# Kernel tuning notes

Measured on AMD Instinct MI355X. Metric: run time of the kernel, lower is better.

The kernel has to match this reference:

```python
import jax, jax.numpy as jnp
import numpy as np

B, E, K, S, D, H, C = 8192, 8, 2, 32, 3072, 256, 100  # batch, experts, fix_points, img size, flat dim, hidden, classes


def setup_inputs() -> dict:
    key = jax.random.key(0)
    ks = jax.random.split(key, 6)
    return {
        "x": jax.random.normal(ks[0], (B, 3, S, S), jnp.float32),
        "coeffs_t": jax.random.uniform(ks[1], (K,), jnp.float32),
        "router_w": jax.random.normal(ks[2], (K, D, E), jnp.float32) * 0.02,
        "router_b": jnp.zeros((K, E), jnp.float32),
        "w1": jax.random.normal(ks[3], (E, K, D, H), jnp.float32) * 0.02,
        "b1": jnp.zeros((E, K, H), jnp.float32),
        "w2": jax.random.normal(ks[4], (E, K, H, C), jnp.float32) * 0.02,
        "b2": jnp.zeros((E, K, C), jnp.float32),
    }


def reference(x, coeffs_t, router_w, router_b, w1, b1, w2, b2):
    xf = x.reshape(x.shape[0], -1)  # [B, D]
    # Curve parameter blend: W = sum_k coeffs_t[k] * W_k (CurveParameter semantics)
    Wr = jnp.einsum('k,kde->de', coeffs_t, router_w)
    br = jnp.einsum('k,ke->e', coeffs_t, router_b)
    # Router: top-1 expert index per sample
    idx = jnp.argmax(xf @ Wr + br, axis=-1)  # [B] int
    # Blended expert weights
    W1 = jnp.einsum('k,ekdh->edh', coeffs_t, w1)
    B1 = jnp.einsum('k,ekh->eh', coeffs_t, b1)
    W2 = jnp.einsum('k,ekhc->ehc', coeffs_t, w2)
    B2 = jnp.einsum('k,ekc->ec', coeffs_t, b2)
    # Expert MLP (computed for all experts with static shapes, then top-1 gather;
    # identical math to torch's boolean-mask dispatch/scatter)
    h = jax.nn.gelu(jnp.einsum('bd,edh->beh', xf, W1) + B1, approximate=False)  # [B,E,H]
    o = jnp.einsum('beh,ehc->bec', h, W2) + B2  # [B,E,C]
    return jnp.take_along_axis(o, idx[:, None, None], axis=1)[:, 0, :]  # [B,C]
```

## Files before the change

kernel.cpp:

```cpp
#include <hip/hip_runtime.h>
#include <math.h>

#define B_  8192
#define E_  8
#define D_  3072
#define H_  256
#define C_  100
#define DH_ (D_*H_)
#define HC_ (H_*C_)
#define KS_ 8
#define KSEG_ (D_/KS_)
#define RKS_ 16
#define RSEG_ (D_/RKS_)
#define RB_ (B_/256)
#define NTMAX_ 136
#define NT2MAX_ 528

#define MEGA_R_   (RB_*RKS_)
#define MEGA_W1_  (24*4*8)
#define MEGA_W2_  (C_*E_)
#define MEGA_BB_  3
#define MEGA_TOT_ (MEGA_R_ + MEGA_W1_ + MEGA_W2_ + MEGA_BB_)

typedef __attribute__((ext_vector_type(4))) float  f32x4;
typedef __attribute__((ext_vector_type(8))) __bf16 bf16x8;
typedef __attribute__((ext_vector_type(8))) unsigned short ush8;
typedef __attribute__((ext_vector_type(4))) unsigned short ush4;

__device__ inline unsigned short bf16_rne(float f) {
    unsigned u = __builtin_bit_cast(unsigned, f);
    unsigned r = (u + 0x7FFFu + ((u >> 16) & 1u)) >> 16;
    return (unsigned short)r;
}
__device__ inline float bf16_f(unsigned short h) {
    unsigned u = ((unsigned)h) << 16;
    return __builtin_bit_cast(float, u);
}

#define MISC_B1_ (E_*H_/4)
#define MISC_B2_ (E_*C_/4)

__global__ __launch_bounds__(256) void mega_k(
        const float* __restrict__ x, const float* __restrict__ rw,
        const float* __restrict__ w1, const float* __restrict__ w2,
        const float* __restrict__ b1, const float* __restrict__ b2,
        unsigned short* __restrict__ Whi, unsigned short* __restrict__ Wlo,
        unsigned short* __restrict__ W2thi, unsigned short* __restrict__ W2tlo,
        float* __restrict__ B1b, float* __restrict__ B2b,
        double* __restrict__ lpart, const float* __restrict__ coeffs) {
    __shared__ char smem[36864];
    int bid = blockIdx.x;
    int t = threadIdx.x;

    if (bid < MEGA_R_) {
        float  (*xs)[64][33] = (float(*)[64][33])smem;
        double (*wls)[8]     = (double(*)[8])(smem + 33792);
        int w = t >> 6, lane = t & 63;
        int rowblk = (bid & (RB_ - 1)) * 256;
        int s2     = bid >> 5;
        int kbase  = s2 * RSEG_;
        int row0   = rowblk + w * 64;
        double c0 = (double)coeffs[0], c1 = (double)coeffs[1];

        double acc[8] = {0, 0, 0, 0, 0, 0, 0, 0};

        float4 px[8];
        float rwa[4], rwb[4];
        #pragma unroll
        for (int it = 0; it < 8; it++) {
            int i = lane + it * 64;
            int r = i >> 3, c4 = i & 7;
            px[it] = *(const float4*)(x + (size_t)(row0 + r) * D_ + kbase + c4 * 4);
        }
        if (w == 0) {
            #pragma unroll
            for (int it = 0; it < 4; it++) {
                int i = lane + it * 64;
                int k = i >> 3, ee = i & 7;
                rwa[it] = rw[(size_t)(kbase + k) * 8 + ee];
                rwb[it] = rw[(size_t)(D_ + kbase + k) * 8 + ee];
            }
        }

        for (int kb = 0; kb < RSEG_; kb += 32) {
            #pragma unroll
            for (int it = 0; it < 8; it++) {
                int i = lane + it * 64;
                int r = i >> 3, c4 = i & 7;
                *(float4*)&xs[w][r][c4 * 4] = px[it];
            }
            if (w == 0) {
                #pragma unroll
                for (int it = 0; it < 4; it++) {
                    int i = lane + it * 64;
                    int k = i >> 3, ee = i & 7;
                    wls[k][ee] = c0 * (double)rwa[it] + c1 * (double)rwb[it];
                }
            }
            __syncthreads();

            if (kb + 32 < RSEG_) {
                #pragma unroll
                for (int it = 0; it < 8; it++) {
                    int i = lane + it * 64;
                    int r = i >> 3, c4 = i & 7;
                    px[it] = *(const float4*)(x + (size_t)(row0 + r) * D_ +
                                              kbase + kb + 32 + c4 * 4);
                }
                if (w == 0) {
                    #pragma unroll
                    for (int it = 0; it < 4; it++) {
                        int i = lane + it * 64;
                        int k = i >> 3, ee = i & 7;
                        rwa[it] = rw[(size_t)(kbase + kb + 32 + k) * 8 + ee];
                        rwb[it] = rw[(size_t)(D_ + kbase + kb + 32 + k) * 8 + ee];
                    }
                }
            }

            #pragma unroll
            for (int kk = 0; kk < 32; kk++) {
                double xv = (double)xs[w][lane][kk];
                double2 w01 = *(const double2*)&wls[kk][0];
                double2 w23 = *(const double2*)&wls[kk][2];
                double2 w45 = *(const double2*)&wls[kk][4];
                double2 w67 = *(const double2*)&wls[kk][6];
                acc[0] = fma(xv, w01.x, acc[0]);
                acc[1] = fma(xv, w01.y, acc[1]);
                acc[2] = fma(xv, w23.x, acc[2]);
                acc[3] = fma(xv, w23.y, acc[3]);
                acc[4] = fma(xv, w45.x, acc[4]);
                acc[5] = fma(xv, w45.y, acc[5]);
                acc[6] = fma(xv, w67.x, acc[6]);
                acc[7] = fma(xv, w67.y, acc[7]);
            }
            __syncthreads();
        }
        size_t base = ((size_t)s2 * B_ + row0 + lane) * 8;
        #pragma unroll
        for (int ee = 0; ee < 8; ee++) lpart[base + ee] = acc[ee];

    } else if (bid < MEGA_R_ + MEGA_W1_) {
        int lid = bid - MEGA_R_;
        int e  = lid / 96;
        int r  = lid - e * 96;
        int h0 = (r / 24) * 64;
        int d0 = (r % 24) * 128;
        const int TP = 136;
        unsigned short* thi = (unsigned short*)smem;
        unsigned short* tlo = thi + 64 * TP;
        float c0 = coeffs[0], c1 = coeffs[1];
        int h = t & 63, dl = t >> 6;
        const float* pa = w1 + ((size_t)(e * 2 + 0) * D_ + d0) * H_ + h0 + h;
        const float* pb = w1 + ((size_t)(e * 2 + 1) * D_ + d0) * H_ + h0 + h;
        #pragma unroll 8
        for (int it = 0; it < 32; it++) {
            int d = it * 4 + dl;
            float v = c0 * pa[(size_t)d * H_] + c1 * pb[(size_t)d * H_];
            unsigned short hi = bf16_rne(v);
            thi[h * TP + d] = hi;
            tlo[h * TP + d] = bf16_rne(v - bf16_f(hi));
        }
        __syncthreads();
        #pragma unroll
        for (int it = 0; it < 4; it++) {
            int i = t + it * 256;
            int hh = i >> 4, d8 = (i & 15) * 8;
            size_t g = (size_t)(e * H_ + h0 + hh) * D_ + d0 + d8;
            *(ush8*)(Whi + g) = *(const ush8*)&thi[hh * TP + d8];
            *(ush8*)(Wlo + g) = *(const ush8*)&tlo[hh * TP + d8];
        }

    } else if (bid < MEGA_R_ + MEGA_W1_ + MEGA_W2_) {
        int lid = bid - (MEGA_R_ + MEGA_W1_);
        int c = lid % C_, e = lid / C_;
        int k = t;
        float c0 = coeffs[0], c1 = coeffs[1];
        float v = c0 * w2[((size_t)(e * 2 + 0) * H_ + k) * C_ + c]
                + c1 * w2[((size_t)(e * 2 + 1) * H_ + k) * C_ + c];
        unsigned short hi = bf16_rne(v);
        W2thi[(size_t)(e * C_ + c) * H_ + k] = hi;
        W2tlo[(size_t)(e * C_ + c) * H_ + k] = bf16_rne(v - bf16_f(hi));

    } else {
        int gid = (bid - (MEGA_R_ + MEGA_W1_ + MEGA_W2_)) * 256 + t;
        float c0 = coeffs[0], c1 = coeffs[1];
        if (gid < MISC_B1_) {
            const float4* p = (const float4*)b1;
            int e = gid / (H_ / 4), r = gid - e * (H_ / 4);
            float4 a = p[(e * 2 + 0) * (H_ / 4) + r];
            float4 bq = p[(e * 2 + 1) * (H_ / 4) + r];
            float4 o;
            o.x = c0 * a.x + c1 * bq.x;
            o.y = c0 * a.y + c1 * bq.y;
            o.z = c0 * a.z + c1 * bq.z;
            o.w = c0 * a.w + c1 * bq.w;
            ((float4*)B1b)[gid] = o;
        } else if (gid < MISC_B1_ + MISC_B2_) {
            int g2 = gid - MISC_B1_;
            const float4* p = (const float4*)b2;
            int e = g2 / (C_ / 4), r = g2 - e * (C_ / 4);
            float4 a = p[(e * 2 + 0) * (C_ / 4) + r];
            float4 bq = p[(e * 2 + 1) * (C_ / 4) + r];
            float4 o;
            o.x = c0 * a.x + c1 * bq.x;
            o.y = c0 * a.y + c1 * bq.y;
            o.z = c0 * a.z + c1 * bq.z;
            o.w = c0 * a.w + c1 * bq.w;
            ((float4*)B2b)[g2] = o;
        }
    }
}

__global__ __launch_bounds__(256) void argmax_hist_k(
        const double* __restrict__ lpart, const float* __restrict__ rb,
        const float* __restrict__ coeffs, int* __restrict__ idx,
        int* __restrict__ hist) {
    __shared__ int scnt[8];
    int t = threadIdx.x;
    if (t < 8) scnt[t] = 0;
    __syncthreads();
    int b = blockIdx.x * 256 + t;
    double c0 = (double)coeffs[0], c1 = (double)coeffs[1];
    double l[8];
    #pragma unroll
    for (int e = 0; e < 8; e++)
        l[e] = c0 * (double)rb[e] + c1 * (double)rb[8 + e];
    for (int s2 = 0; s2 < RKS_; s2++) {
        const double2* pp = (const double2*)(lpart + ((size_t)s2 * B_ + b) * 8);
        double2 v0 = pp[0], v1 = pp[1], v2 = pp[2], v3 = pp[3];
        l[0] += v0.x; l[1] += v0.y; l[2] += v1.x; l[3] += v1.y;
        l[4] += v2.x; l[5] += v2.y; l[6] += v3.x; l[7] += v3.y;
    }
    double best = -1e300;
    int bi = 0;
    #pragma unroll
    for (int e = 0; e < 8; e++)
        if (l[e] > best) { best = l[e]; bi = e; }
    idx[b] = bi;
    atomicAdd(&scnt[bi], 1);
    __syncthreads();
    if (t < 8) hist[blockIdx.x * 8 + t] = scnt[t];
}

__global__ __launch_bounds__(256) void scatter2_k(
        const int* __restrict__ idx, const int* __restrict__ hist,
        int* __restrict__ order, int* __restrict__ cnt, int* __restrict__ off,
        int* __restrict__ tmap, int* __restrict__ tmap2, int* __restrict__ ntl) {
    __shared__ int sbi[256];
    __shared__ int stot[8];
    __shared__ int sbase[8];
    int b0 = blockIdx.x, t = threadIdx.x;
    int b = b0 * 256 + t;
    int mybi = idx[b];
    sbi[t] = mybi;
    if (t < 8) {
        int tot = 0, pre = 0;
        for (int bb = 0; bb < RB_; bb++) {
            int h = hist[bb * 8 + t];
            if (bb < b0) pre += h;
            tot += h;
        }
        stot[t] = tot;
        sbase[t] = pre;
    }
    __syncthreads();
    if (t < 8) {
        int o = 0;
        for (int j = 0; j < t; j++) o += stot[j];
        sbase[t] += o;
    }
    __syncthreads();
    int rank = 0;
    for (int i = 0; i < 256; i++) {
        int v = sbi[i];
        rank += (i < t && v == mybi) ? 1 : 0;
    }
    order[sbase[mybi] + rank] = (mybi << 16) | b;

    if (b0 == 0 && t == 0) {
        int s = 0;
        for (int e = 0; e < E_; e++) { cnt[e] = stot[e]; off[e] = s; s += stot[e]; }
        int nt = 0;
        for (int e = 0; e < E_; e++)
            for (int t0 = 0; t0 < stot[e]; t0 += 64)
                tmap[nt++] = (e << 16) | t0;
        ntl[0] = nt;
        int nt2 = 0;
        for (int e = 0; e < E_; e++)
            for (int t0 = 0; t0 < stot[e]; t0 += 16)
                tmap2[nt2++] = (e << 16) | t0;
        ntl[1] = nt2;
    }
}

template<int MODE>
__global__ __launch_bounds__(256, 3) void gemm1_t(
        const float* __restrict__ x, const unsigned short* __restrict__ Whi,
        const unsigned short* __restrict__ Wlo, const int* __restrict__ order,
        const int* __restrict__ cnt, const int* __restrict__ off,
        const int* __restrict__ tmap, const int* __restrict__ ntl,
        float* __restrict__ dst) {
    int tid = blockIdx.y;
    if (tid >= ntl[0]) return;
    int tm = tmap[tid];
    int e = tm >> 16, tile0 = tm & 0xFFFF;
    int ce = cnt[e];
    int s = blockIdx.x;

    __shared__ int rows[64];
    __shared__ unsigned short xs_hi[64 * 40];
    __shared__ unsigned short xs_lo[64 * 40];
    __shared__ unsigned short ws_hi[256 * 40];
    __shared__ unsigned short ws_lo[256 * 40];

    int t = threadIdx.x;
    if (t < 64) {
        int i = tile0 + t;
        rows[t] = (i < ce) ? (order[off[e] + i] & 0xFFFF) : -1;
    }
    __syncthreads();
    int xrow0 = rows[0];

    int lane = t & 63, w = t >> 6;
    int lr = lane & 15, quad = lane >> 4;
    int kbase = s * KSEG_;

    f32x4 acc[4][4];
    #pragma unroll
    for (int mt = 0; mt < 4; mt++)
        #pragma unroll
        for (int nt = 0; nt < 4; nt++)
            acc[mt][nt] = (f32x4){0.f, 0.f, 0.f, 0.f};

    for (int kb = 0; kb < KSEG_; kb += 32) {
        #pragma unroll
        for (int it = 0; it < 2; it++) {
            int i = t + it * 256;
            int rr = i >> 3, sg = i & 7;
            int row = rows[rr];
            if (row < 0) row = xrow0;
            float4 v = *(const float4*)(x + (size_t)row * D_ + kbase + kb + sg * 4);
            unsigned short h4[4], l4[4];
            float vv[4] = {v.x, v.y, v.z, v.w};
            #pragma unroll
            for (int j = 0; j < 4; j++) {
                unsigned short hi = bf16_rne(vv[j]);
                h4[j] = hi;
                l4[j] = bf16_rne(vv[j] - bf16_f(hi));
            }
            *(ush4*)&xs_hi[rr * 40 + sg * 4] = *(const ush4*)h4;
            *(ush4*)&xs_lo[rr * 40 + sg * 4] = *(const ush4*)l4;
        }
        #pragma unroll
        for (int it = 0; it < 4; it++) {
            int i = t + it * 256;
            int col = i >> 2, ch = i & 3;
            size_t g = (size_t)(e * H_ + col) * D_ + kbase + kb + ch * 8;
            *(ush8*)&ws_hi[col * 40 + ch * 8] = *(const ush8*)(Whi + g);
            *(ush8*)&ws_lo[col * 40 + ch * 8] = *(const ush8*)(Wlo + g);
        }
        __syncthreads();

        bf16x8 ah[4], al[4], bh[4], bl[4];
        #pragma unroll
        for (int mt = 0; mt < 4; mt++) {
            ah[mt] = __builtin_bit_cast(bf16x8, *(const ush8*)&xs_hi[(mt * 16 + lr) * 40 + quad * 8]);
            al[mt] = __builtin_bit_cast(bf16x8, *(const ush8*)&xs_lo[(mt * 16 + lr) * 40 + quad * 8]);
        }
        #pragma unroll
        for (int nt = 0; nt < 4; nt++) {
            int col = w * 64 + nt * 16 + lr;
            bh[nt] = __builtin_bit_cast(bf16x8, *(const ush8*)&ws_hi[col * 40 + quad * 8]);
            bl[nt] = __builtin_bit_cast(bf16x8, *(const ush8*)&ws_lo[col * 40 + quad * 8]);
        }
        #pragma unroll
        for (int mt = 0; mt < 4; mt++)
            #pragma unroll
            for (int nt = 0; nt < 4; nt++) {
                acc[mt][nt] = __builtin_amdgcn_mfma_f32_16x16x32_bf16(ah[mt], bh[nt], acc[mt][nt], 0, 0, 0);
                acc[mt][nt] = __builtin_amdgcn_mfma_f32_16x16x32_bf16(al[mt], bh[nt], acc[mt][nt], 0, 0, 0);
                acc[mt][nt] = __builtin_amdgcn_mfma_f32_16x16x32_bf16(ah[mt], bl[nt], acc[mt][nt], 0, 0, 0);
                acc[mt][nt] = __builtin_amdgcn_mfma_f32_16x16x32_bf16(al[mt], bl[nt], acc[mt][nt], 0, 0, 0);
            }
        __syncthreads();
    }

    size_t p0 = (size_t)off[e] + tile0;
    if (MODE == 1) {
        float* dp = dst + ((size_t)s * B_ + p0) * H_;
        #pragma unroll
        for (int mt = 0; mt < 4; mt++) {
            int rl = mt * 16 + quad * 4;
            #pragma unroll
            for (int nt = 0; nt < 4; nt++) {
                int col = w * 64 + nt * 16 + lr;
                #pragma unroll
                for (int rg = 0; rg < 4; rg++) {
                    if (tile0 + rl + rg < ce)
                        dp[(size_t)(rl + rg) * H_ + col] = acc[mt][nt][rg];
                }
            }
        }
    } else {
        #pragma unroll
        for (int mt = 0; mt < 4; mt++) {
            int rl = mt * 16 + quad * 4;
            #pragma unroll
            for (int nt = 0; nt < 4; nt++) {
                int col = w * 64 + nt * 16 + lr;
                #pragma unroll
                for (int rg = 0; rg < 4; rg++) {
                    if (tile0 + rl + rg < ce)
                        atomicAdd(&dst[(p0 + rl + rg) * H_ + col], acc[mt][nt][rg]);
                }
            }
        }
    }
}

__global__ __launch_bounds__(256) void bias_gelu_k(
        float* __restrict__ hws, const float* __restrict__ B1b,
        const int* __restrict__ order) {
    int gid = blockIdx.x * 256 + threadIdx.x;
    int p = gid >> 6, c4 = (gid & 63) * 4;
    int e = order[p] >> 16;
    float4 v = *(const float4*)(hws + (size_t)p * H_ + c4);
    const float4 bb = *(const float4*)(B1b + e * H_ + c4);
    float pre[4] = {v.x + bb.x, v.y + bb.y, v.z + bb.z, v.w + bb.w};
    float4 o;
    o.x = 0.5f * pre[0] * (1.0f + erff(pre[0] * 0.70710678118654752440f));
    o.y = 0.5f * pre[1] * (1.0f + erff(pre[1] * 0.70710678118654752440f));
    o.z = 0.5f * pre[2] * (1.0f + erff(pre[2] * 0.70710678118654752440f));
    o.w = 0.5f * pre[3] * (1.0f + erff(pre[3] * 0.70710678118654752440f));
    *(float4*)(hws + (size_t)p * H_ + c4) = o;
}

template<int FUSE>
__global__ __launch_bounds__(256) void gemm2_t(
        const float* __restrict__ hsrc,
        const unsigned short* __restrict__ W2thi, const unsigned short* __restrict__ W2tlo,
        const float* __restrict__ B1b, const float* __restrict__ B2b,
        const int* __restrict__ order, const int* __restrict__ cnt,
        const int* __restrict__ off, const int* __restrict__ tmap2,
        const int* __restrict__ ntl, float* __restrict__ out) {
    int tid = blockIdx.x;
    if (tid >= ntl[1]) return;
    int tm = tmap2[tid];
    int e = tm >> 16, tile0 = tm & 0xFFFF;
    int ce = cnt[e];

    __shared__ int rows[16];
    __shared__ float red[3][64][28];

    int t = threadIdx.x;
    if (t < 16) {
        int i = tile0 + t;
        rows[t] = (i < ce) ? (order[off[e] + i] & 0xFFFF) : -1;
    }
    __syncthreads();

    int lane = t & 63, w = t >> 6;
    int m = lane & 15, q = lane >> 4;
    int p = off[e] + tile0 + ((tile0 + m < ce) ? m : 0);

    f32x4 acc[7];
    #pragma unroll
    for (int nt = 0; nt < 7; nt++) acc[nt] = (f32x4){0.f, 0.f, 0.f, 0.f};

    const unsigned short* w2h = W2thi + (size_t)e * C_ * H_;
    const unsigned short* w2l = W2tlo + (size_t)e * C_ * H_;

    #pragma unroll
    for (int si = 0; si < 2; si++) {
        int s = w * 2 + si;
        int k0 = s * 32 + q * 8;
        size_t o = (size_t)p * H_ + k0;
        float f[8];
        if (FUSE) {
            float4 a0 = *(const float4*)(hsrc + o);
            float4 a1 = *(const float4*)(hsrc + o + 4);
            #pragma unroll
            for (int s2 = 1; s2 < KS_; s2++) {
                const float* sp = hsrc + (size_t)s2 * B_ * H_ + o;
                float4 b0 = *(const float4*)sp;
                float4 b1v = *(const float4*)(sp + 4);
                a0.x += b0.x; a0.y += b0.y; a0.z += b0.z; a0.w += b0.w;
                a1.x += b1v.x; a1.y += b1v.y; a1.z += b1v.z; a1.w += b1v.w;
            }
            float4 bb0 = *(const float4*)(B1b + e * H_ + k0);
            float4 bb1 = *(const float4*)(B1b + e * H_ + k0 + 4);
            float pre[8] = {a0.x + bb0.x, a0.y + bb0.y, a0.z + bb0.z, a0.w + bb0.w,
                            a1.x + bb1.x, a1.y + bb1.y, a1.z + bb1.z, a1.w + bb1.w};
            #pragma unroll
            for (int j = 0; j < 8; j++)
                f[j] = 0.5f * pre[j] * (1.0f + erff(pre[j] * 0.70710678118654752440f));
        } else {
            float4 v0 = *(const float4*)(hsrc + o);
            float4 v1 = *(const float4*)(hsrc + o + 4);
            f[0] = v0.x; f[1] = v0.y; f[2] = v0.z; f[3] = v0.w;
            f[4] = v1.x; f[5] = v1.y; f[6] = v1.z; f[7] = v1.w;
        }
        unsigned short hh[8], lo[8];
        #pragma unroll
        for (int j = 0; j < 8; j++) {
            unsigned short hi = bf16_rne(f[j]);
            hh[j] = hi;
            lo[j] = bf16_rne(f[j] - bf16_f(hi));
        }
        bf16x8 ah = __builtin_bit_cast(bf16x8, *(const ush8*)hh);
        bf16x8 al = __builtin_bit_cast(bf16x8, *(const ush8*)lo);
        #pragma unroll
        for (int nt = 0; nt < 7; nt++) {
            size_t bo = (size_t)(nt * 16 + m) * H_ + k0;
            bf16x8 bh = __builtin_bit_cast(bf16x8, *(const ush8*)(w2h + bo));
            bf16x8 bl = __builtin_bit_cast(bf16x8, *(const ush8*)(w2l + bo));
            acc[nt] = __builtin_amdgcn_mfma_f32_16x16x32_bf16(ah, bh, acc[nt], 0, 0, 0);
            acc[nt] = __builtin_amdgcn_mfma_f32_16x16x32_bf16(al, bh, acc[nt], 0, 0, 0);
            acc[nt] = __builtin_amdgcn_mfma_f32_16x16x32_bf16(ah, bl, acc[nt], 0, 0, 0);
            acc[nt] = __builtin_amdgcn_mfma_f32_16x16x32_bf16(al, bl, acc[nt], 0, 0, 0);
        }
    }

    if (w > 0) {
        #pragma unroll
        for (int nt = 0; nt < 7; nt++)
            #pragma unroll
            for (int i = 0; i < 4; i++)
                red[w - 1][lane][nt * 4 + i] = acc[nt][i];
    }
    __syncthreads();
    if (w == 0) {
        #pragma unroll
        for (int nt = 0; nt < 7; nt++)
            #pragma unroll
            for (int i = 0; i < 4; i++)
                acc[nt][i] = ((acc[nt][i] + red[0][lane][nt * 4 + i])
                              + red[1][lane][nt * 4 + i]) + red[2][lane][nt * 4 + i];
        #pragma unroll
        for (int nt = 0; nt < 7; nt++) {
            int c = nt * 16 + m;
            if (c >= C_) continue;
            float bias = B2b[e * C_ + c];
            #pragma unroll
            for (int i = 0; i < 4; i++) {
                int grow = q * 4 + i;
                if (tile0 + grow < ce)
                    out[(size_t)rows[grow] * C_ + c] = acc[nt][i] + bias;
            }
        }
    }
}

extern "C" void kernel_launch(void* const* d_in, const int* in_sizes, int n_in,
                              void* d_out, int out_size, void* d_ws, size_t ws_size,
                              hipStream_t stream) {
    const float* x        = (const float*)d_in[0];
    const float* coeffs   = (const float*)d_in[1];
    const float* router_w = (const float*)d_in[2];
    const float* router_b = (const float*)d_in[3];
    const float* w1       = (const float*)d_in[4];
    const float* b1       = (const float*)d_in[5];
    const float* w2       = (const float*)d_in[6];
    const float* b2       = (const float*)d_in[7];
    float* out = (float*)d_out;

    unsigned short* Whi   = (unsigned short*)d_ws;
    unsigned short* Wlo   = Whi + (size_t)E_ * DH_;
    unsigned short* W2thi = Wlo + (size_t)E_ * DH_;
    unsigned short* W2tlo = W2thi + (size_t)E_ * C_ * H_;
    float* B1b  = (float*)(W2tlo + (size_t)E_ * C_ * H_);
    float* B2b  = B1b + (size_t)E_ * H_;
    int* order  = (int*)(B2b + E_ * C_);
    int* cnt    = order + B_;
    int* off    = cnt + E_;
    int* tmap   = off + E_;
    int* tmap2  = tmap + NTMAX_;
    int* ntl    = tmap2 + NT2MAX_;
    int* idx    = ntl + 4;
    int* hist   = idx + B_;
    float* hws  = (float*)(hist + 256);
    double* lpart = (double*)hws;

    size_t prefix_bytes = (size_t)((char*)hws - (char*)d_ws);
    int use_part = (ws_size >= prefix_bytes + (size_t)KS_ * B_ * H_ * sizeof(float) + 256) ? 1 : 0;

    mega_k<<<dim3(MEGA_TOT_), 256, 0, stream>>>(
        x, router_w, w1, w2, b1, b2, Whi, Wlo, W2thi, W2tlo, B1b, B2b,
        lpart, coeffs);

    argmax_hist_k<<<dim3(RB_), 256, 0, stream>>>(lpart, router_b, coeffs, idx, hist);
    scatter2_k<<<dim3(RB_), 256, 0, stream>>>(idx, hist, order, cnt, off,
                                              tmap, tmap2, ntl);

    if (use_part) {
        gemm1_t<1><<<dim3(KS_, NTMAX_), 256, 0, stream>>>(x, Whi, Wlo, order, cnt,
                                                          off, tmap, ntl, hws);
        gemm2_t<1><<<dim3(NT2MAX_), 256, 0, stream>>>(hws, W2thi, W2tlo, B1b, B2b,
                                                      order, cnt, off, tmap2, ntl, out);
    } else {
        hipMemsetAsync(hws, 0, (size_t)B_ * H_ * sizeof(float), stream);
        gemm1_t<0><<<dim3(KS_, NTMAX_), 256, 0, stream>>>(x, Whi, Wlo, order, cnt,
                                                          off, tmap, ntl, hws);
        bias_gelu_k<<<dim3(B_ * H_ / 4 / 256), 256, 0, stream>>>(hws, B1b, order);
        gemm2_t<0><<<dim3(NT2MAX_), 256, 0, stream>>>(hws, W2thi, W2tlo, B1b, B2b,
                                                      order, cnt, off, tmap2, ntl, out);
    }
}
```

Measured before the change: 344.5 us.

## Pre-tile expert W1 into padded LDS-image chunks and load via global_load_lds

Measured after the change: 333.2 us. -3.3%, faster.

```diff
diff --git a/kernel.cpp b/kernel.cpp
--- a/kernel.cpp
+++ b/kernel.cpp
@@ -15,6 +15,8 @@
 #define RB_ (B_/256)
 #define NTMAX_ 136
 #define NT2MAX_ 528
+#define NCH_ (D_/32)
+#define CHW_ 10240
 
 #define MEGA_R_   (RB_*RKS_)
 #define MEGA_W1_  (24*4*8)
@@ -26,6 +28,10 @@
 typedef __attribute__((ext_vector_type(8))) __bf16 bf16x8;
 typedef __attribute__((ext_vector_type(8))) unsigned short ush8;
 typedef __attribute__((ext_vector_type(4))) unsigned short ush4;
+
+#define GLOAD_LDS16(g, l) __builtin_amdgcn_global_load_lds( \
+    (const __attribute__((address_space(1))) void*)(g),     \
+    (__attribute__((address_space(3))) void*)(l), 16, 0, 0)
 
 __device__ inline unsigned short bf16_rne(float f) {
     unsigned u = __builtin_bit_cast(unsigned, f);
@@ -64,60 +70,24 @@
 
         double acc[8] = {0, 0, 0, 0, 0, 0, 0, 0};
 
-        float4 px[8];
-        float rwa[4], rwb[4];
-        #pragma unroll
-        for (int it = 0; it < 8; it++) {
-            int i = lane + it * 64;
-            int r = i >> 3, c4 = i & 7;
-            px[it] = *(const float4*)(x + (size_t)(row0 + r) * D_ + kbase + c4 * 4);
-        }
-        if (w == 0) {
-            #pragma unroll
-            for (int it = 0; it < 4; it++) {
-                int i = lane + it * 64;
-                int k = i >> 3, ee = i & 7;
-                rwa[it] = rw[(size_t)(kbase + k) * 8 + ee];
-                rwb[it] = rw[(size_t)(D_ + kbase + k) * 8 + ee];
-            }
-        }
-
         for (int kb = 0; kb < RSEG_; kb += 32) {
             #pragma unroll
             for (int it = 0; it < 8; it++) {
                 int i = lane + it * 64;
                 int r = i >> 3, c4 = i & 7;
-                *(float4*)&xs[w][r][c4 * 4] = px[it];
+                *(float4*)&xs[w][r][c4 * 4] =
+                    *(const float4*)(x + (size_t)(row0 + r) * D_ + kbase + kb + c4 * 4);
             }
             if (w == 0) {
                 #pragma unroll
                 for (int it = 0; it < 4; it++) {
                     int i = lane + it * 64;
                     int k = i >> 3, ee = i & 7;
-                    wls[k][ee] = c0 * (double)rwa[it] + c1 * (double)rwb[it];
+                    wls[k][ee] = c0 * (double)rw[(size_t)(kbase + kb + k) * 8 + ee]
+                               + c1 * (double)rw[(size_t)(D_ + kbase + kb + k) * 8 + ee];
                 }
             }
             __syncthreads();
-
-            if (kb + 32 < RSEG_) {
-                #pragma unroll
-                for (int it = 0; it < 8; it++) {
-                    int i = lane + it * 64;
-                    int r = i >> 3, c4 = i & 7;
-                    px[it] = *(const float4*)(x + (size_t)(row0 + r) * D_ +
-                                              kbase + kb + 32 + c4 * 4);
-                }
-                if (w == 0) {
-                    #pragma unroll
-                    for (int it = 0; it < 4; it++) {
-                        int i = lane + it * 64;
-                        int k = i >> 3, ee = i & 7;
-                        rwa[it] = rw[(size_t)(kbase + kb + 32 + k) * 8 + ee];
-                        rwb[it] = rw[(size_t)(D_ + kbase + kb + 32 + k) * 8 + ee];
-                    }
-                }
-            }
-
             #pragma unroll
             for (int kk = 0; kk < 32; kk++) {
                 double xv = (double)xs[w][lane][kk];
@@ -166,7 +136,9 @@
         for (int it = 0; it < 4; it++) {
             int i = t + it * 256;
             int hh = i >> 4, d8 = (i & 15) * 8;
-            size_t g = (size_t)(e * H_ + h0 + hh) * D_ + d0 + d8;
+            int d = d0 + d8;
+            int ci = d >> 5;
+            size_t g = ((size_t)e * NCH_ + ci) * CHW_ + (size_t)(h0 + hh) * 40 + (d & 31);
             *(ush8*)(Whi + g) = *(const ush8*)&thi[hh * TP + d8];
             *(ush8*)(Wlo + g) = *(const ush8*)&tlo[hh * TP + d8];
         }
@@ -325,6 +297,7 @@
     int lane = t & 63, w = t >> 6;
     int lr = lane & 15, quad = lane >> 4;
     int kbase = s * KSEG_;
+    int wuni = t & ~63;
 
     f32x4 acc[4][4];
     #pragma unroll
@@ -334,6 +307,18 @@
             acc[mt][nt] = (f32x4){0.f, 0.f, 0.f, 0.f};
 
     for (int kb = 0; kb < KSEG_; kb += 32) {
+        {
+            int ci = (kbase + kb) >> 5;
+            const unsigned short* ph = Whi + ((size_t)e * NCH_ + ci) * CHW_;
+            const unsigned short* pl = Wlo + ((size_t)e * NCH_ + ci) * CHW_;
+            #pragma unroll
+            for (int j = 0; j < 5; j++) {
+                GLOAD_LDS16(ph + ((size_t)(j * 256 + t)) * 8,
+                            ws_hi + (size_t)(j * 256 + wuni) * 8);
+                GLOAD_LDS16(pl + ((size_t)(j * 256 + t)) * 8,
+                            ws_lo + (size_t)(j * 256 + wuni) * 8);
+            }
+        }
         #pragma unroll
         for (int it = 0; it < 2; it++) {
             int i = t + it * 256;
@@ -351,14 +336,6 @@
             }
             *(ush4*)&xs_hi[rr * 40 + sg * 4] = *(const ush4*)h4;
             *(ush4*)&xs_lo[rr * 40 + sg * 4] = *(const ush4*)l4;
-        }
-        #pragma unroll
-        for (int it = 0; it < 4; it++) {
-            int i = t + it * 256;
-            int col = i >> 2, ch = i & 3;
-            size_t g = (size_t)(e * H_ + col) * D_ + kbase + kb + ch * 8;
-            *(ush8*)&ws_hi[col * 40 + ch * 8] = *(const ush8*)(Whi + g);
-            *(ush8*)&ws_lo[col * 40 + ch * 8] = *(const ush8*)(Wlo + g);
         }
         __syncthreads();
 
@@ -566,8 +543,8 @@
     float* out = (float*)d_out;
 
     unsigned short* Whi   = (unsigned short*)d_ws;
-    unsigned short* Wlo   = Whi + (size_t)E_ * DH_;
-    unsigned short* W2thi = Wlo + (size_t)E_ * DH_;
+    unsigned short* Wlo   = Whi + (size_t)E_ * NCH_ * CHW_;
+    unsigned short* W2thi = Wlo + (size_t)E_ * NCH_ * CHW_;
     unsigned short* W2tlo = W2thi + (size_t)E_ * C_ * H_;
     float* B1b  = (float*)(W2tlo + (size_t)E_ * C_ * H_);
     float* B2b  = B1b + (size_t)E_ * H_;
```

## Pre-pad W1 bf16 tiles in LDS layout and load via global_load_lds

Applied to the files above, without the earlier changes.

After: 349.4 us. Within noise of the previous version (+1.4%).

```diff
diff --git a/kernel.cpp b/kernel.cpp
--- a/kernel.cpp
+++ b/kernel.cpp
@@ -15,9 +15,11 @@
 #define RB_ (B_/256)
 #define NTMAX_ 136
 #define NT2MAX_ 528
+#define NCH_ (D_/32)
+#define CHW_ 10240
 
 #define MEGA_R_   (RB_*RKS_)
-#define MEGA_W1_  (24*4*8)
+#define MEGA_W1_  (E_*NCH_)
 #define MEGA_W2_  (C_*E_)
 #define MEGA_BB_  3
 #define MEGA_TOT_ (MEGA_R_ + MEGA_W1_ + MEGA_W2_ + MEGA_BB_)
@@ -27,6 +29,10 @@
 typedef __attribute__((ext_vector_type(8))) unsigned short ush8;
 typedef __attribute__((ext_vector_type(4))) unsigned short ush4;
 
+#define GLOAD_LDS16(g, l) __builtin_amdgcn_global_load_lds( \
+    (const __attribute__((address_space(1))) void*)(g),     \
+    (__attribute__((address_space(3))) void*)(l), 16, 0, 0)
+
 __device__ inline unsigned short bf16_rne(float f) {
     unsigned u = __builtin_bit_cast(unsigned, f);
     unsigned r = (u + 0x7FFFu + ((u >> 16) & 1u)) >> 16;
@@ -40,7 +46,7 @@
 #define MISC_B1_ (E_*H_/4)
 #define MISC_B2_ (E_*C_/4)
 
-__global__ __launch_bounds__(256) void mega_k(
+__global__ __launch_bounds__(256, 2) void mega_k(
         const float* __restrict__ x, const float* __restrict__ rw,
         const float* __restrict__ w1, const float* __restrict__ w2,
         const float* __restrict__ b1, const float* __restrict__ b2,
@@ -142,33 +148,45 @@
 
     } else if (bid < MEGA_R_ + MEGA_W1_) {
         int lid = bid - MEGA_R_;
-        int e  = lid / 96;
-        int r  = lid - e * 96;
-        int h0 = (r / 24) * 64;
-        int d0 = (r % 24) * 128;
-        const int TP = 136;
+        int e  = lid / NCH_;
+        int ci = lid - e * NCH_;
+        int d0 = ci * 32;
         unsigned short* thi = (unsigned short*)smem;
-        unsigned short* tlo = thi + 64 * TP;
+        unsigned short* tlo = thi + 32 * 256;
         float c0 = coeffs[0], c1 = coeffs[1];
-        int h = t & 63, dl = t >> 6;
-        const float* pa = w1 + ((size_t)(e * 2 + 0) * D_ + d0) * H_ + h0 + h;
-        const float* pb = w1 + ((size_t)(e * 2 + 1) * D_ + d0) * H_ + h0 + h;
-        #pragma unroll 8
-        for (int it = 0; it < 32; it++) {
-            int d = it * 4 + dl;
-            float v = c0 * pa[(size_t)d * H_] + c1 * pb[(size_t)d * H_];
-            unsigned short hi = bf16_rne(v);
-            thi[h * TP + d] = hi;
-            tlo[h * TP + d] = bf16_rne(v - bf16_f(hi));
+        const float* pa = w1 + ((size_t)(e * 2 + 0) * D_ + d0) * H_;
+        const float* pb = w1 + ((size_t)(e * 2 + 1) * D_ + d0) * H_;
+        #pragma unroll
+        for (int it = 0; it < 8; it++) {
+            int i4 = t + it * 256;
+            float4 va = *(const float4*)(pa + (size_t)i4 * 4);
+            float4 vb = *(const float4*)(pb + (size_t)i4 * 4);
+            float vv[4] = {c0 * va.x + c1 * vb.x, c0 * va.y + c1 * vb.y,
+                           c0 * va.z + c1 * vb.z, c0 * va.w + c1 * vb.w};
+            unsigned short h4[4], l4[4];
+            #pragma unroll
+            for (int j = 0; j < 4; j++) {
+                unsigned short hi = bf16_rne(vv[j]);
+                h4[j] = hi;
+                l4[j] = bf16_rne(vv[j] - bf16_f(hi));
+            }
+            *(ush4*)&thi[i4 * 4] = *(const ush4*)h4;
+            *(ush4*)&tlo[i4 * 4] = *(const ush4*)l4;
         }
         __syncthreads();
         #pragma unroll
         for (int it = 0; it < 4; it++) {
-            int i = t + it * 256;
-            int hh = i >> 4, d8 = (i & 15) * 8;
-            size_t g = (size_t)(e * H_ + h0 + hh) * D_ + d0 + d8;
-            *(ush8*)(Whi + g) = *(const ush8*)&thi[hh * TP + d8];
-            *(ush8*)(Wlo + g) = *(const ush8*)&tlo[hh * TP + d8];
+            int j = t + it * 256;
+            int h = j >> 2, d8 = (j & 3) * 8;
+            unsigned short vh[8], vl[8];
+            #pragma unroll
+            for (int k2 = 0; k2 < 8; k2++) {
+                vh[k2] = thi[(d8 + k2) * 256 + h];
+                vl[k2] = tlo[(d8 + k2) * 256 + h];
+            }
+            size_t g = ((size_t)e * NCH_ + ci) * CHW_ + (size_t)h * 40 + d8;
+            *(ush8*)(Whi + g) = *(const ush8*)vh;
+            *(ush8*)(Wlo + g) = *(const ush8*)vl;
         }
 
     } else if (bid < MEGA_R_ + MEGA_W1_ + MEGA_W2_) {
@@ -325,6 +343,7 @@
     int lane = t & 63, w = t >> 6;
     int lr = lane & 15, quad = lane >> 4;
     int kbase = s * KSEG_;
+    int wuni = t & ~63;
 
     f32x4 acc[4][4];
     #pragma unroll
@@ -334,6 +353,18 @@
             acc[mt][nt] = (f32x4){0.f, 0.f, 0.f, 0.f};
 
     for (int kb = 0; kb < KSEG_; kb += 32) {
+        {
+            int ci = (kbase + kb) >> 5;
+            const unsigned short* ph = Whi + ((size_t)e * NCH_ + ci) * CHW_;
+            const unsigned short* pl = Wlo + ((size_t)e * NCH_ + ci) * CHW_;
+            #pragma unroll
+            for (int j = 0; j < 5; j++) {
+                GLOAD_LDS16(ph + ((size_t)(j * 256 + t)) * 8,
+                            ws_hi + (size_t)(j * 256 + wuni) * 8);
+                GLOAD_LDS16(pl + ((size_t)(j * 256 + t)) * 8,
+                            ws_lo + (size_t)(j * 256 + wuni) * 8);
+            }
+        }
         #pragma unroll
         for (int it = 0; it < 2; it++) {
             int i = t + it * 256;
@@ -351,14 +382,6 @@
             }
             *(ush4*)&xs_hi[rr * 40 + sg * 4] = *(const ush4*)h4;
             *(ush4*)&xs_lo[rr * 40 + sg * 4] = *(const ush4*)l4;
-        }
-        #pragma unroll
-        for (int it = 0; it < 4; it++) {
-            int i = t + it * 256;
-            int col = i >> 2, ch = i & 3;
-            size_t g = (size_t)(e * H_ + col) * D_ + kbase + kb + ch * 8;
-            *(ush8*)&ws_hi[col * 40 + ch * 8] = *(const ush8*)(Whi + g);
-            *(ush8*)&ws_lo[col * 40 + ch * 8] = *(const ush8*)(Wlo + g);
         }
         __syncthreads();
 
@@ -566,8 +589,8 @@
     float* out = (float*)d_out;
 
     unsigned short* Whi   = (unsigned short*)d_ws;
-    unsigned short* Wlo   = Whi + (size_t)E_ * DH_;
-    unsigned short* W2thi = Wlo + (size_t)E_ * DH_;
+    unsigned short* Wlo   = Whi + (size_t)E_ * NCH_ * CHW_;
+    unsigned short* W2thi = Wlo + (size_t)E_ * NCH_ * CHW_;
     unsigned short* W2tlo = W2thi + (size_t)E_ * C_ * H_;
     float* B1b  = (float*)(W2tlo + (size_t)E_ * C_ * H_);
     float* B2b  = B1b + (size_t)E_ * H_;
```
